# Performance work log

Hardware: AMD Instinct MI355X
Metric: run time of the kernel (lower is better)

Reference implementation:

```python
import jax, jax.numpy as jnp
import numpy as np
from jax.scipy.special import logsumexp

NEG_INF = -1e9


def _lstm(x, wih, whh, bih, bhh):
    # x: [B, L, D] -> (hs [B, L, H], h_last [B, H]); PyTorch gate order i,f,g,o
    B = x.shape[0]
    H = whh.shape[1]
    def step(carry, xt):
        h, c = carry
        g = xt @ wih.T + h @ whh.T + bih + bhh
        i, f, gg, o = jnp.split(g, 4, axis=-1)
        c = jax.nn.sigmoid(f) * c + jax.nn.sigmoid(i) * jnp.tanh(gg)
        h = jax.nn.sigmoid(o) * jnp.tanh(c)
        return (h, c), h
    init = (jnp.zeros((B, H), x.dtype), jnp.zeros((B, H), x.dtype))
    (hT, _), hs = jax.lax.scan(step, init, jnp.swapaxes(x, 0, 1))
    return jnp.swapaxes(hs, 0, 1), hT


def _forward(word_ids, char_ids, mask, tags, p):
    (word_emb, char_emb_cnn, conv_w3, conv_b3, conv_w5, conv_b5, conv_w7, conv_b7,
     char_emb_lstm, cl_wih_f, cl_whh_f, cl_bih_f, cl_bhh_f,
     cl_wih_b, cl_whh_b, cl_bih_b, cl_bhh_b,
     fuse_w, fuse_b,
     ctx_wih_f, ctx_whh_f, ctx_bih_f, ctx_bhh_f,
     ctx_wih_b, ctx_whh_b, ctx_bih_b, ctx_bhh_b,
     attn_w, attn_b, attn_v, emis_w, emis_b,
     crf_start, crf_end, crf_trans) = p
    B, T = word_ids.shape
    Wc = char_ids.shape[2]
    we = word_emb[word_ids]                                    # [B,T,200]
    cids = char_ids.reshape(B * T, Wc)
    # --- Char CNN branch: conv1d(relu) + max-over-time per kernel size ---
    ce = jnp.swapaxes(char_emb_cnn[cids], 1, 2)                # [BT,30,W]
    feats = []
    for w, b in ((conv_w3, conv_b3), (conv_w5, conv_b5), (conv_w7, conv_b7)):
        k = w.shape[-1]
        y = jax.lax.conv_general_dilated(ce, w, (1,), [(k // 2, k // 2)],
                                         dimension_numbers=('NCW', 'OIW', 'NCW'))
        feats.append(jnp.max(jax.nn.relu(y + b[None, :, None]), axis=2))
    cnn_feat = jnp.concatenate(feats, axis=1).reshape(B, T, -1)    # [B,T,96]
    # --- Char BiLSTM branch: final hidden states of both directions ---
    cel = char_emb_lstm[cids]                                  # [BT,W,30]
    _, hf = _lstm(cel, cl_wih_f, cl_whh_f, cl_bih_f, cl_bhh_f)
    _, hb = _lstm(cel[:, ::-1], cl_wih_b, cl_whh_b, cl_bih_b, cl_bhh_b)
    lstm_feat = jnp.concatenate([hf, hb], axis=1).reshape(B, T, -1)  # [B,T,100]
    # --- Fusion (dropout is identity in eval) ---
    combined = jnp.concatenate([we, cnn_feat, lstm_feat], axis=-1)   # [B,T,396]
    fused = jax.nn.relu(combined @ fuse_w.T + fuse_b)                # [B,T,200]
    # --- Context BiLSTM ---
    hs_f, _ = _lstm(fused, ctx_wih_f, ctx_whh_f, ctx_bih_f, ctx_bhh_f)
    hs_b, _ = _lstm(fused[:, ::-1], ctx_wih_b, ctx_whh_b, ctx_bih_b, ctx_bhh_b)
    H = jnp.concatenate([hs_f, hs_b[:, ::-1]], axis=-1)              # [B,T,256]
    # --- Token attention ---
    scores = jnp.tanh(H @ attn_w.T + attn_b) @ attn_v                # [B,T]
    scores = jnp.where(mask, scores, NEG_INF)
    H = H * jax.nn.softmax(scores, axis=1)[..., None]
    emis = H @ emis_w.T + emis_b                                     # [B,T,K]
    # --- CRF negative mean log-likelihood (time-major) ---
    em = jnp.swapaxes(emis, 0, 1)                                    # [T,B,K]
    m = jnp.swapaxes(mask, 0, 1).astype(em.dtype)                    # [T,B]
    tg = jnp.swapaxes(tags, 0, 1)                                    # [T,B]
    barange = jnp.arange(B)
    emit = jnp.take_along_axis(em, tg[:, :, None], axis=2)[:, :, 0]  # [T,B]
    trans_sc = crf_trans[tg[:-1], tg[1:]]                            # [T-1,B]
    num = crf_start[tg[0]] + emit[0] + jnp.sum((trans_sc + emit[1:]) * m[1:], axis=0)
    last_idx = m.sum(axis=0).astype(jnp.int32) - 1
    num = num + crf_end[tg[last_idx, barange]]
    def crf_step(alpha, inp):
        e_t, m_t = inp
        nxt = logsumexp(alpha[:, :, None] + crf_trans[None] + e_t[:, None, :], axis=1)
        return jnp.where(m_t[:, None] > 0, nxt, alpha), None
    alpha, _ = jax.lax.scan(crf_step, crf_start + em[0], (em[1:], m[1:]))
    logZ = logsumexp(alpha + crf_end, axis=1)                        # [B]
    return -(num - logZ).mean()


def setup_inputs() -> dict:
    key = jax.random.key(0)
    ks = iter(jax.random.split(key, 64))
    def rn(shape, s=0.1):
        return jax.random.normal(next(ks), shape, jnp.float32) * s
    B, T, Wc, V, Cv, K = 64, 256, 16, 100000, 100, 9
    return dict(
        word_ids=jax.random.randint(next(ks), (B, T), 0, V),
        char_ids=jax.random.randint(next(ks), (B, T, Wc), 0, Cv),
        mask=jnp.ones((B, T), bool),
        tags=jax.random.randint(next(ks), (B, T), 0, K),
        word_emb=rn((V, 200)),
        char_emb_cnn=rn((Cv, 30)),
        conv_w3=rn((32, 30, 3)), conv_b3=rn((32,)),
        conv_w5=rn((32, 30, 5)), conv_b5=rn((32,)),
        conv_w7=rn((32, 30, 7)), conv_b7=rn((32,)),
        char_emb_lstm=rn((Cv, 30)),
        cl_wih_f=rn((200, 30)), cl_whh_f=rn((200, 50)), cl_bih_f=rn((200,)), cl_bhh_f=rn((200,)),
        cl_wih_b=rn((200, 30)), cl_whh_b=rn((200, 50)), cl_bih_b=rn((200,)), cl_bhh_b=rn((200,)),
        fuse_w=rn((200, 396)), fuse_b=rn((200,)),
        ctx_wih_f=rn((512, 200)), ctx_whh_f=rn((512, 128)), ctx_bih_f=rn((512,)), ctx_bhh_f=rn((512,)),
        ctx_wih_b=rn((512, 200)), ctx_whh_b=rn((512, 128)), ctx_bih_b=rn((512,)), ctx_bhh_b=rn((512,)),
        attn_w=rn((256, 256)), attn_b=rn((256,)), attn_v=rn((256,)),
        emis_w=rn((K, 256)), emis_b=rn((K,)),
        crf_start=rn((K,)), crf_end=rn((K,)), crf_trans=rn((K, K)),
    )


def reference(word_ids, char_ids, mask, tags, word_emb, char_emb_cnn, conv_w3, conv_b3, conv_w5, conv_b5, conv_w7, conv_b7, char_emb_lstm, cl_wih_f, cl_whh_f, cl_bih_f, cl_bhh_f, cl_wih_b, cl_whh_b, cl_bih_b, cl_bhh_b, fuse_w, fuse_b, ctx_wih_f, ctx_whh_f, ctx_bih_f, ctx_bhh_f, ctx_wih_b, ctx_whh_b, ctx_bih_b, ctx_bhh_b, attn_w, attn_b, attn_v, emis_w, emis_b, crf_start, crf_end, crf_trans):
    p = (word_emb, char_emb_cnn, conv_w3, conv_b3, conv_w5, conv_b5, conv_w7, conv_b7,
         char_emb_lstm, cl_wih_f, cl_whh_f, cl_bih_f, cl_bhh_f,
         cl_wih_b, cl_whh_b, cl_bih_b, cl_bhh_b,
         fuse_w, fuse_b,
         ctx_wih_f, ctx_whh_f, ctx_bih_f, ctx_bhh_f,
         ctx_wih_b, ctx_whh_b, ctx_bih_b, ctx_bhh_b,
         attn_w, attn_b, attn_v, emis_w, emis_b,
         crf_start, crf_end, crf_trans)
    return _forward(word_ids, char_ids, mask, tags, p)
```

## Files before the change

kernel.cpp:

```cpp
#include <hip/hip_runtime.h>
#include <hip/hip_fp16.h>

#define NB_B 64
#define NT 256
#define NWC 16

__device__ __forceinline__ float sigf(float x){ return 1.0f/(1.0f + __expf(-x)); }
__device__ __forceinline__ float tanhf_(float x){ return 1.0f - 2.0f/(__expf(2.0f*x)+1.0f); }

typedef _Float16 h2_t __attribute__((ext_vector_type(2)));

__device__ __forceinline__ float dot2f(unsigned int w, unsigned int x, float acc){
#if __has_builtin(__builtin_amdgcn_fdot2)
  return __builtin_amdgcn_fdot2(__builtin_bit_cast(h2_t, w), __builtin_bit_cast(h2_t, x), acc, false);
#else
  h2_t a = __builtin_bit_cast(h2_t, w), b = __builtin_bit_cast(h2_t, x);
  return acc + (float)a[0]*(float)b[0] + (float)a[1]*(float)b[1];
#endif
}

__device__ __forceinline__ unsigned int packh2(float a, float b){
  return ((unsigned int)__half_as_ushort(__float2half(a))) |
         (((unsigned int)__half_as_ushort(__float2half(b))) << 16);
}


__global__ void k_transpose(const float* __restrict__ src, float* __restrict__ dst, int R, int C){
  int idx = blockIdx.x*256 + threadIdx.x;
  if (idx < R*C){ int r = idx / C, c = idx % C; dst[c*R + r] = src[idx]; }
}

__global__ void k_prep_ctx(const float* __restrict__ wih_f, const float* __restrict__ whh_f,
                           const float* __restrict__ bih_f, const float* __restrict__ bhh_f,
                           const float* __restrict__ wih_b, const float* __restrict__ whh_b,
                           const float* __restrict__ bih_b, const float* __restrict__ bhh_b,
                           unsigned int* __restrict__ wihP, unsigned int* __restrict__ whhQ,
                           float* __restrict__ biasc){
  int idx = blockIdx.x*256 + threadIdx.x;
  const int NIH = 2*100*512, NHH = 2*16*512*4;
  if (idx < NIH){
    int dir = idx / (100*512); int r = idx % (100*512); int k = r >> 9; int j = r & 511;
    const float* wih = dir ? wih_b : wih_f;
    wihP[idx] = packh2(wih[j*200 + 2*k], wih[j*200 + 2*k + 1]);
  } else if (idx < NIH + NHH){
    int i2 = idx - NIH;
    int dir = i2 / 32768; int r = i2 % 32768;
    int k4 = r / 2048; int r2 = r % 2048; int j = r2 >> 2; int e = r2 & 3;
    const float* whh = dir ? whh_b : whh_f;
    whhQ[i2] = packh2(whh[j*128 + 8*k4 + 2*e], whh[j*128 + 8*k4 + 2*e + 1]);
  } else if (idx < NIH + NHH + 1024){
    int i2 = idx - NIH - NHH; int dir = i2 >> 9; int j = i2 & 511;
    biasc[i2] = dir ? (bih_b[j] + bhh_b[j]) : (bih_f[j] + bhh_f[j]);
  }
}

__global__ void k_prep_P4(const float* __restrict__ emb,
                          const float* __restrict__ wih_f, const float* __restrict__ bih_f, const float* __restrict__ bhh_f,
                          const float* __restrict__ wih_b, const float* __restrict__ bih_b, const float* __restrict__ bhh_b,
                          float4* __restrict__ P4){
  int idx = blockIdx.x*256 + threadIdx.x;
  if (idx >= 10000) return;
  int dir = idx / 5000; int r = idx % 5000; int c = r / 50; int u = r % 50;
  const float* wih = dir ? wih_b : wih_f;
  const float* bih = dir ? bih_b : bih_f;
  const float* bhh = dir ? bhh_b : bhh_f;
  float g4[4];
  #pragma unroll
  for (int gt = 0; gt < 4; gt++){
    int j = gt*50 + u;
    float acc = bih[j] + bhh[j];
    for (int k = 0; k < 30; k++) acc += emb[c*30 + k] * wih[j*30 + k];
    g4[gt] = acc;
  }
  P4[idx] = make_float4(g4[0], g4[1], g4[2], g4[3]);
}

__global__ void k_prep_whh2(const float* __restrict__ whh_f, const float* __restrict__ whh_b,
                            unsigned int* __restrict__ W2){
  int idx = blockIdx.x*256 + threadIdx.x;
  if (idx >= 10000) return;
  int dir = idx / 5000; int r = idx % 5000;
  int u = r / 100; int r2 = r % 100; int gt = r2 / 25; int k = r2 % 25;
  const float* whh = dir ? whh_b : whh_f;
  int j = gt*50 + u;
  W2[idx] = packh2(whh[j*50 + 2*k], whh[j*50 + 2*k + 1]);
}

__global__ void k_prep_Q(const float* __restrict__ emb, const float* __restrict__ w3,
                         const float* __restrict__ w5, const float* __restrict__ w7,
                         float* __restrict__ Q){
  int idx = blockIdx.x*256 + threadIdx.x;
  if (idx >= 48000) return;
  const float* w; int ks, r;
  if (idx < 9600){ w = w3; ks = 3; r = idx; }
  else if (idx < 25600){ w = w5; ks = 5; r = idx - 9600; }
  else { w = w7; ks = 7; r = idx - 25600; }
  int t = r / 3200; int o = (r / 100) % 32; int c = r % 100;
  float acc = 0.f;
  for (int i = 0; i < 30; i++) acc += emb[c*30 + i] * w[(o*30 + i)*ks + t];
  Q[idx] = acc;
}


__global__ void k_gather(const int* __restrict__ word_ids, const float* __restrict__ word_emb,
                         float* __restrict__ combined){
  int idx = blockIdx.x*256 + threadIdx.x;
  if (idx >= NB_B*NT*200) return;
  int bt = idx / 200; int k = idx - bt*200;
  combined[bt*396 + k] = word_emb[(long)word_ids[bt]*200 + k];
}

template<int KS>
__global__ __launch_bounds__(512) void k_cnn2(const int* __restrict__ char_ids,
                                              const float* __restrict__ Qg,
                                              const float* __restrict__ bias,
                                              float* __restrict__ combined,
                                              int outoff){
  constexpr int PAD = KS/2;
  const int tid = threadIdx.x;
  __shared__ float Qlds[KS*3200];
  for (int idx = tid; idx < KS*3200; idx += 512){
    int t = idx / 3200; int r = idx - t*3200; int cc = r >> 5; int oo = r & 31;
    Qlds[idx] = Qg[(t*32 + oo)*100 + cc];
  }
  __syncthreads();
  const int o    = tid & 31;
  const int word = blockIdx.x*16 + ((tid >> 6) << 1) + ((tid >> 5) & 1);
  int ch[16];
  #pragma unroll
  for (int p = 0; p < 16; p++) ch[p] = char_ids[word*16 + p];
  float m = -1e30f;
  #pragma unroll
  for (int p = 0; p < 16; p++){
    float acc = 0.f;
    #pragma unroll
    for (int t = 0; t < KS; t++){
      int pp = p + t - PAD;
      if (pp >= 0 && pp < 16) acc += Qlds[(t*100 + ch[pp])*32 + o];
    }
    m = fmaxf(m, acc);
  }
  combined[(long)word*396 + 200 + outoff + o] = fmaxf(m + bias[o], 0.f);
}

__global__ __launch_bounds__(320, 2) void k_char_lstm(const int* __restrict__ char_ids,
                                                      const float4* __restrict__ P4,
                                                      const unsigned int* __restrict__ W2,
                                                      float* __restrict__ combined){
  const int lane = threadIdx.x & 63;
  const int g10  = __builtin_amdgcn_readfirstlane(threadIdx.x >> 6);
  const int word = blockIdx.x*64 + lane;
  const int dir  = blockIdx.y;
  const float4* __restrict__ P4d = P4 + dir*5000;
  const unsigned int* __restrict__ W2d = W2 + dir*5000 + g10*1000;

  __shared__ unsigned int hbuf[2][64*27];

  int ch[16];
  #pragma unroll
  for (int p = 0; p < 16; p++) ch[p] = char_ids[word*16 + p];

  float c[10], hval[10];
  #pragma unroll
  for (int u = 0; u < 10; u++){ c[u] = 0.f; hval[u] = 0.f; }
  for (int i = threadIdx.x; i < 64*27; i += 320) hbuf[0][i] = 0u;
  __syncthreads();

  #pragma unroll 1
  for (int t = 0; t < 16; t++){
    const int p = t & 1;
    const int cid = ch[dir ? (15 - t) : t];
    float4 pg[10];
    #pragma unroll
    for (int u = 0; u < 10; u++) pg[u] = P4d[cid*50 + g10*10 + u];
    unsigned int hp[25];
    #pragma unroll
    for (int k = 0; k < 25; k++) hp[k] = hbuf[p][lane*27 + k];
    #pragma unroll 2
    for (int u = 0; u < 10; u++){
      const unsigned int* __restrict__ wr = W2d + u*100;
      float ai = pg[u].x, af = pg[u].y, ag = pg[u].z, ao = pg[u].w;
      #pragma unroll
      for (int k = 0; k < 25; k++){
        ai = dot2f(wr[k],      hp[k], ai);
        af = dot2f(wr[25 + k], hp[k], af);
        ag = dot2f(wr[50 + k], hp[k], ag);
        ao = dot2f(wr[75 + k], hp[k], ao);
      }
      c[u] = sigf(af)*c[u] + sigf(ai)*tanhf_(ag);
      hval[u] = sigf(ao)*tanhf_(c[u]);
    }
    #pragma unroll
    for (int i = 0; i < 5; i++)
      hbuf[1-p][lane*27 + g10*5 + i] = packh2(hval[2*i], hval[2*i+1]);
    __syncthreads();
  }
  #pragma unroll
  for (int u = 0; u < 10; u++)
    combined[(long)word*396 + 296 + dir*50 + g10*10 + u] = hval[u];
}

__global__ __launch_bounds__(256) void k_fuse(const float* __restrict__ combined,
                                              const float* __restrict__ wFT,
                                              const float* __restrict__ fb,
                                              float* __restrict__ fused){
  int tid = threadIdx.x; int base = blockIdx.x*4;
  __shared__ float rows[4*396];
  for (int idx = tid; idx < 4*396; idx += 256) rows[idx] = combined[(long)base*396 + idx];
  __syncthreads();
  if (tid < 200){
    float a0=0.f, a1=0.f, a2=0.f, a3=0.f;
    #pragma unroll 4
    for (int k = 0; k < 396; k++){
      float w = wFT[k*200 + tid];
      a0 += w*rows[k]; a1 += w*rows[396+k]; a2 += w*rows[792+k]; a3 += w*rows[1188+k];
    }
    float bb = fb[tid];
    fused[(base+0)*200 + tid] = fmaxf(a0 + bb, 0.f);
    fused[(base+1)*200 + tid] = fmaxf(a1 + bb, 0.f);
    fused[(base+2)*200 + tid] = fmaxf(a2 + bb, 0.f);
    fused[(base+3)*200 + tid] = fmaxf(a3 + bb, 0.f);
  }
}

__global__ __launch_bounds__(512) void k_gx(const float* __restrict__ fused,
                                            const unsigned int* __restrict__ wihP,
                                            const float* __restrict__ biasc,
                                            __half* __restrict__ Gx){
  const int dir = blockIdx.y, j = threadIdx.x;
  const int base = blockIdx.x*8;
  __shared__ __align__(16) unsigned int xh[8*100];
  for (int idx = j; idx < 800; idx += 512){
    int r = idx / 100, k = idx - r*100;
    const float2* fr2 = (const float2*)(fused + (long)(base + r)*200);
    float2 v = fr2[k];
    xh[r*100 + k] = packh2(v.x, v.y);
  }
  __syncthreads();
  float acc[8];
  float bj = biasc[dir*512 + j];
  #pragma unroll
  for (int r = 0; r < 8; r++) acc[r] = bj;
  const unsigned int* wp = wihP + dir*(100*512) + j;
  #pragma unroll 1
  for (int kk = 0; kk < 25; kk++){
    unsigned int w0 = wp[(4*kk+0)*512];
    unsigned int w1 = wp[(4*kk+1)*512];
    unsigned int w2 = wp[(4*kk+2)*512];
    unsigned int w3 = wp[(4*kk+3)*512];
    #pragma unroll
    for (int r = 0; r < 8; r++){
      uint4 xv = *(const uint4*)&xh[r*100 + kk*4];
      float a = acc[r];
      a = dot2f(w0, xv.x, a);
      a = dot2f(w1, xv.y, a);
      a = dot2f(w2, xv.z, a);
      a = dot2f(w3, xv.w, a);
      acc[r] = a;
    }
  }
  #pragma unroll
  for (int r = 0; r < 8; r++)
    Gx[((long)dir*16384 + base + r)*512 + j] = __float2half(acc[r]);
}

__global__ __launch_bounds__(512) void k_ctx_rec(const __half* __restrict__ Gx,
                                                 const uint4* __restrict__ whhQ,
                                                 __half* __restrict__ H){
  const int b = blockIdx.x, dir = blockIdx.y, j = threadIdx.x;
  __shared__ __align__(16) unsigned int hh[64];
  __shared__ float gs[512];
  float c = 0.f;
  if (j < 64) hh[j] = 0u;
  __syncthreads();
  const __half* gx_base = Gx + ((long)dir*16384 + b*256)*512;
  const uint4* wq = whhQ + dir*(16*512) + j;

  #pragma unroll 1
  for (int t = 0; t < 256; t++){
    int tsrc = dir ? (255 - t) : t;
    float acc = __half2float(gx_base[(long)tsrc*512 + j]);
    const uint4* hq = (const uint4*)hh;
    #pragma unroll
    for (int k4 = 0; k4 < 16; k4++){
      uint4 w = wq[k4*512];
      uint4 hv = hq[k4];
      acc = dot2f(w.x, hv.x, acc);
      acc = dot2f(w.y, hv.y, acc);
      acc = dot2f(w.z, hv.z, acc);
      acc = dot2f(w.w, hv.w, acc);
    }
    gs[j] = acc;
    __syncthreads();
    if (j < 128){
      float gi = gs[j], gf = gs[j+128], gg = gs[j+256], go = gs[j+384];
      c = sigf(gf)*c + sigf(gi)*tanhf_(gg);
      float hv = sigf(go)*tanhf_(c);
      H[((long)b*256 + tsrc)*256 + dir*128 + j] = __float2half(hv);
      ((unsigned short*)hh)[j] = __half_as_ushort(__float2half(hv));
    }
    __syncthreads();
  }
}


__global__ __launch_bounds__(256) void k_attn(const __half* __restrict__ H,
                                              const float* __restrict__ attnT,
                                              const float* __restrict__ attn_b,
                                              const float* __restrict__ attn_v,
                                              float* __restrict__ scores){
  int tid = threadIdx.x; int base = blockIdx.x*4;
  __shared__ float rows[4*256];
  __shared__ float red[4*256];
  for (int idx = tid; idx < 1024; idx += 256) rows[idx] = __half2float(H[(long)base*256 + idx]);
  __syncthreads();
  float a0=0.f, a1=0.f, a2=0.f, a3=0.f;
  #pragma unroll 4
  for (int k = 0; k < 256; k++){
    float w = attnT[k*256 + tid];
    a0 += w*rows[k]; a1 += w*rows[256+k]; a2 += w*rows[512+k]; a3 += w*rows[768+k];
  }
  float ab = attn_b[tid], av = attn_v[tid];
  red[tid]       = tanhf_(a0 + ab)*av;
  red[256 + tid] = tanhf_(a1 + ab)*av;
  red[512 + tid] = tanhf_(a2 + ab)*av;
  red[768 + tid] = tanhf_(a3 + ab)*av;
  __syncthreads();
  for (int s = 128; s > 0; s >>= 1){
    if (tid < s){
      red[tid] += red[tid+s]; red[256+tid] += red[256+tid+s];
      red[512+tid] += red[512+tid+s]; red[768+tid] += red[768+tid+s];
    }
    __syncthreads();
  }
  if (tid < 4) scores[base + tid] = red[tid*256];
}

__global__ __launch_bounds__(256) void k_softmax(float* __restrict__ scores){
  int b = blockIdx.x, tid = threadIdx.x;
  __shared__ float red[256];
  float s = scores[b*256 + tid];
  red[tid] = s; __syncthreads();
  for (int st = 128; st > 0; st >>= 1){ if (tid < st) red[tid] = fmaxf(red[tid], red[tid+st]); __syncthreads(); }
  float m = red[0]; __syncthreads();
  float e = __expf(s - m);
  red[tid] = e; __syncthreads();
  for (int st = 128; st > 0; st >>= 1){ if (tid < st) red[tid] += red[tid+st]; __syncthreads(); }
  float inv = 1.0f / red[0];
  scores[b*256 + tid] = e * inv;
}

__global__ __launch_bounds__(256) void k_emis(const __half* __restrict__ H, const float* __restrict__ scores,
                                              const float* __restrict__ emis_w, const float* __restrict__ emis_b,
                                              float* __restrict__ emis){
  int tid = threadIdx.x; int base = blockIdx.x*4;
  int r = tid >> 6, j = tid & 63;
  __shared__ float rows[4*256];
  for (int idx = tid; idx < 1024; idx += 256) rows[idx] = __half2float(H[(long)base*256 + idx]);
  __syncthreads();
  if (j < 9){
    float acc = 0.f;
    #pragma unroll 4
    for (int k = 0; k < 256; k++) acc += rows[r*256 + k] * emis_w[j*256 + k];
    int tok = base + r;
    emis[tok*9 + j] = scores[tok]*acc + emis_b[j];
  }
}


__global__ __launch_bounds__(64) void k_crf(const float* __restrict__ emis, const float* __restrict__ trans,
                                            const float* __restrict__ startv, const float* __restrict__ endv,
                                            float* __restrict__ logZ){
  int b = blockIdx.x; int j = threadIdx.x;
  bool act = (j < 9);
  float alpha = act ? (startv[j] + emis[(b*256)*9 + j]) : -1e30f;
  float trow[9];
  #pragma unroll
  for (int i = 0; i < 9; i++) trow[i] = act ? trans[i*9 + j] : 0.f;
  for (int t = 1; t < 256; t++){
    float v[9];
    #pragma unroll
    for (int i = 0; i < 9; i++) v[i] = __shfl(alpha, i) + trow[i];
    float m = v[0];
    #pragma unroll
    for (int i = 1; i < 9; i++) m = fmaxf(m, v[i]);
    float ssum = 0.f;
    #pragma unroll
    for (int i = 0; i < 9; i++) ssum += expf(v[i] - m);
    float e = act ? emis[(b*256 + t)*9 + j] : 0.f;
    alpha = m + logf(ssum) + e;
  }
  float v = act ? (alpha + endv[j]) : -1e30f;
  float vv[9];
  float m = -1e30f;
  #pragma unroll
  for (int i = 0; i < 9; i++){ vv[i] = __shfl(v, i); m = fmaxf(m, vv[i]); }
  float ssum = 0.f;
  #pragma unroll
  for (int i = 0; i < 9; i++) ssum += expf(vv[i] - m);
  if (j == 0) logZ[b] = m + logf(ssum);
}

__global__ __launch_bounds__(256) void k_num(const int* __restrict__ tags, const float* __restrict__ emis,
                                             const float* __restrict__ trans, const float* __restrict__ startv,
                                             const float* __restrict__ endv, float* __restrict__ num){
  int b = blockIdx.x, t = threadIdx.x;
  int tg = tags[b*256 + t];
  float v = emis[(b*256 + t)*9 + tg];
  if (t > 0) v += trans[tags[b*256 + t - 1]*9 + tg];
  __shared__ float red[256];
  red[t] = v; __syncthreads();
  for (int s = 128; s > 0; s >>= 1){ if (t < s) red[t] += red[t+s]; __syncthreads(); }
  if (t == 0) num[b] = red[0] + startv[tags[b*256]] + endv[tags[b*256 + 255]];
}

__global__ __launch_bounds__(64) void k_final(const float* __restrict__ logZ, const float* __restrict__ num,
                                              float* __restrict__ out){
  int b = threadIdx.x;
  float v = logZ[b] - num[b];
  for (int s = 32; s > 0; s >>= 1) v += __shfl_down(v, s);
  if (b == 0) out[0] = v * (1.0f/64.0f);
}

__global__ void k_diag(float* __restrict__ out, float ws_mb){
  if (threadIdx.x == 0) out[0] = -ws_mb;
}


extern "C" void kernel_launch(void* const* d_in, const int* in_sizes, int n_in,
                              void* d_out, int out_size, void* d_ws, size_t ws_size,
                              hipStream_t stream) {
  const int*   word_ids   = (const int*)  d_in[0];
  const int*   char_ids   = (const int*)  d_in[1];
  const int*   tags       = (const int*)  d_in[3];
  const float* word_emb   = (const float*)d_in[4];
  const float* emb_cnn    = (const float*)d_in[5];
  const float* conv_w3    = (const float*)d_in[6];
  const float* conv_b3    = (const float*)d_in[7];
  const float* conv_w5    = (const float*)d_in[8];
  const float* conv_b5    = (const float*)d_in[9];
  const float* conv_w7    = (const float*)d_in[10];
  const float* conv_b7    = (const float*)d_in[11];
  const float* emb_lstm   = (const float*)d_in[12];
  const float* cl_wih_f   = (const float*)d_in[13];
  const float* cl_whh_f   = (const float*)d_in[14];
  const float* cl_bih_f   = (const float*)d_in[15];
  const float* cl_bhh_f   = (const float*)d_in[16];
  const float* cl_wih_b   = (const float*)d_in[17];
  const float* cl_whh_b   = (const float*)d_in[18];
  const float* cl_bih_b   = (const float*)d_in[19];
  const float* cl_bhh_b   = (const float*)d_in[20];
  const float* fuse_w     = (const float*)d_in[21];
  const float* fuse_b     = (const float*)d_in[22];
  const float* ctx_wih_f  = (const float*)d_in[23];
  const float* ctx_whh_f  = (const float*)d_in[24];
  const float* ctx_bih_f  = (const float*)d_in[25];
  const float* ctx_bhh_f  = (const float*)d_in[26];
  const float* ctx_wih_b  = (const float*)d_in[27];
  const float* ctx_whh_b  = (const float*)d_in[28];
  const float* ctx_bih_b  = (const float*)d_in[29];
  const float* ctx_bhh_b  = (const float*)d_in[30];
  const float* attn_w     = (const float*)d_in[31];
  const float* attn_b     = (const float*)d_in[32];
  const float* attn_v     = (const float*)d_in[33];
  const float* emis_w     = (const float*)d_in[34];
  const float* emis_b     = (const float*)d_in[35];
  const float* crf_start  = (const float*)d_in[36];
  const float* crf_end    = (const float*)d_in[37];
  const float* crf_trans  = (const float*)d_in[38];
  float* out = (float*)d_out;
  float* ws  = (float*)d_ws;

  const size_t OFF_A      = 0;
  const size_t OFF_FUSED  = 8388608;
  const size_t OFF_SCORES = 11665408;
  const size_t OFF_EMIS   = 11681792;
  const size_t OFF_WIHP   = 11829248;
  const size_t OFF_WHHQ   = 11931648;
  const size_t OFF_BIASC  = 11997184;
  const size_t OFF_P4     = 11998208;
  const size_t OFF_Q      = 12038208;
  const size_t OFF_W2     = 12086208;
  const size_t OFF_WFT    = 12096208;
  const size_t OFF_ATTNT  = 12175408;
  const size_t OFF_NUM    = 12240944;
  const size_t OFF_LOGZ   = 12241008;
  const size_t TOTAL_FLOATS = 12241072;

  if (ws_size < TOTAL_FLOATS * sizeof(float)) {
    k_diag<<<1, 64, 0, stream>>>(out, (float)((double)ws_size / (1024.0*1024.0)));
    return;
  }

  float* combined = ws + OFF_A;
  __half* Gx      = (__half*)(ws + OFF_A);
  float* fused    = ws + OFF_FUSED;
  __half* H       = (__half*)(ws + OFF_FUSED);
  float* scores   = ws + OFF_SCORES;
  float* emis     = ws + OFF_EMIS;
  unsigned int* wihP = (unsigned int*)(ws + OFF_WIHP);
  unsigned int* whhQ = (unsigned int*)(ws + OFF_WHHQ);
  float* biasc    = ws + OFF_BIASC;
  float4* P4      = (float4*)(ws + OFF_P4);
  float* Q        = ws + OFF_Q;
  unsigned int* W2 = (unsigned int*)(ws + OFF_W2);
  float* wFT      = ws + OFF_WFT;
  float* attnT    = ws + OFF_ATTNT;
  float* num      = ws + OFF_NUM;
  float* logZ     = ws + OFF_LOGZ;

  k_transpose<<<(200*396 + 255)/256, 256, 0, stream>>>(fuse_w, wFT, 200, 396);
  k_transpose<<<(256*256 + 255)/256, 256, 0, stream>>>(attn_w, attnT, 256, 256);
  k_prep_ctx<<<(2*100*512 + 2*16*512*4 + 1024 + 255)/256, 256, 0, stream>>>(
      ctx_wih_f, ctx_whh_f, ctx_bih_f, ctx_bhh_f,
      ctx_wih_b, ctx_whh_b, ctx_bih_b, ctx_bhh_b, wihP, whhQ, biasc);
  k_prep_P4<<<(10000 + 255)/256, 256, 0, stream>>>(
      emb_lstm, cl_wih_f, cl_bih_f, cl_bhh_f, cl_wih_b, cl_bih_b, cl_bhh_b, P4);
  k_prep_whh2<<<(10000 + 255)/256, 256, 0, stream>>>(cl_whh_f, cl_whh_b, W2);
  k_prep_Q<<<(48000 + 255)/256, 256, 0, stream>>>(emb_cnn, conv_w3, conv_w5, conv_w7, Q);

  k_gather<<<(NB_B*NT*200 + 255)/256, 256, 0, stream>>>(word_ids, word_emb, combined);
  k_cnn2<3><<<NB_B*NT/16, 512, 0, stream>>>(char_ids, Q,         conv_b3, combined, 0);
  k_cnn2<5><<<NB_B*NT/16, 512, 0, stream>>>(char_ids, Q + 9600,  conv_b5, combined, 32);
  k_cnn2<7><<<NB_B*NT/16, 512, 0, stream>>>(char_ids, Q + 25600, conv_b7, combined, 64);
  k_char_lstm<<<dim3(NB_B*NT/64, 2), 320, 0, stream>>>(char_ids, P4, W2, combined);
  k_fuse<<<NB_B*NT/4, 256, 0, stream>>>(combined, wFT, fuse_b, fused);

  k_gx<<<dim3(NB_B*NT/8, 2), 512, 0, stream>>>(fused, wihP, biasc, Gx);
  k_ctx_rec<<<dim3(NB_B, 2), 512, 0, stream>>>(Gx, (const uint4*)whhQ, H);

  k_attn<<<NB_B*NT/4, 256, 0, stream>>>(H, attnT, attn_b, attn_v, scores);
  k_softmax<<<NB_B, 256, 0, stream>>>(scores);
  k_emis<<<NB_B*NT/4, 256, 0, stream>>>(H, scores, emis_w, emis_b, emis);

  k_crf<<<NB_B, 64, 0, stream>>>(emis, crf_trans, crf_start, crf_end, logZ);
  k_num<<<NB_B, 256, 0, stream>>>(tags, emis, crf_trans, crf_start, crf_end, num);
  k_final<<<1, 64, 0, stream>>>(logZ, num, out);
}
```

Baseline: 1.131 ms.

## Rewrite char BiLSTM recurrence with MFMA 16x16x32 f16 matrix ops

The char-level BiLSTM recurrence now runs on MFMA instructions instead of per-lane fdot2 loops. Each wavefront handles 16 words independently. Recurrent weights are pre-packed into padded f16 B-fragments held in registers, and the input projection table is interleaved per gate so it can seed the accumulator. Gates are redistributed through LDS per wave with no block-wide barriers. The goal is to remove the scalar dot-product cost and the syncthreads per timestep. The price is padding waste (50 to 52 units, 50 to 64 K) and extra LDS round trips.

```diff
diff --git a/kernel.cpp b/kernel.cpp
--- a/kernel.cpp
+++ b/kernel.cpp
@@ -9,6 +9,8 @@
 __device__ __forceinline__ float tanhf_(float x){ return 1.0f - 2.0f/(__expf(2.0f*x)+1.0f); }
 
 typedef _Float16 h2_t __attribute__((ext_vector_type(2)));
+typedef _Float16 f16x8 __attribute__((ext_vector_type(8)));
+typedef float    f32x4 __attribute__((ext_vector_type(4)));
 
 __device__ __forceinline__ float dot2f(unsigned int w, unsigned int x, float acc){
 #if __has_builtin(__builtin_amdgcn_fdot2)
@@ -54,36 +56,41 @@
   }
 }
 
-__global__ void k_prep_P4(const float* __restrict__ emb,
-                          const float* __restrict__ wih_f, const float* __restrict__ bih_f, const float* __restrict__ bhh_f,
-                          const float* __restrict__ wih_b, const float* __restrict__ bih_b, const float* __restrict__ bhh_b,
-                          float4* __restrict__ P4){
+__global__ void k_prep_p4i(const float* __restrict__ emb,
+                           const float* __restrict__ wih_f, const float* __restrict__ bih_f, const float* __restrict__ bhh_f,
+                           const float* __restrict__ wih_b, const float* __restrict__ bih_b, const float* __restrict__ bhh_b,
+                           float* __restrict__ P4I){
   int idx = blockIdx.x*256 + threadIdx.x;
-  if (idx >= 10000) return;
-  int dir = idx / 5000; int r = idx % 5000; int c = r / 50; int u = r % 50;
-  const float* wih = dir ? wih_b : wih_f;
-  const float* bih = dir ? bih_b : bih_f;
-  const float* bhh = dir ? bhh_b : bhh_f;
-  float g4[4];
-  #pragma unroll
-  for (int gt = 0; gt < 4; gt++){
-    int j = gt*50 + u;
+  if (idx >= 41600) return;
+  int n = idx % 208; int cd = idx / 208; int cid = cd % 100; int dir = cd / 100;
+  int u = n >> 2, g = n & 3;
+  float v = 0.f;
+  if (u < 50){
+    int j = g*50 + u;
+    const float* wih = dir ? wih_b : wih_f;
+    const float* bih = dir ? bih_b : bih_f;
+    const float* bhh = dir ? bhh_b : bhh_f;
     float acc = bih[j] + bhh[j];
-    for (int k = 0; k < 30; k++) acc += emb[c*30 + k] * wih[j*30 + k];
-    g4[gt] = acc;
-  }
-  P4[idx] = make_float4(g4[0], g4[1], g4[2], g4[3]);
-}
-
-__global__ void k_prep_whh2(const float* __restrict__ whh_f, const float* __restrict__ whh_b,
-                            unsigned int* __restrict__ W2){
+    for (int k = 0; k < 30; k++) acc += emb[cid*30 + k] * wih[j*30 + k];
+    v = acc;
+  }
+  P4I[idx] = v;
+}
+
+__global__ void k_prep_wb(const float* __restrict__ whh_f, const float* __restrict__ whh_b,
+                          unsigned short* __restrict__ WB){
   int idx = blockIdx.x*256 + threadIdx.x;
-  if (idx >= 10000) return;
-  int dir = idx / 5000; int r = idx % 5000;
-  int u = r / 100; int r2 = r % 100; int gt = r2 / 25; int k = r2 % 25;
+  if (idx >= 26624) return;
+  int e = idx & 7; int l = (idx >> 3) & 63;
+  int dirf = idx >> 9;
+  int dir = dirf / 26; int fr = dirf % 26;
+  int tau = fr >> 1, kh = fr & 1;
+  int n = 16*tau + (l & 15);
+  int u = n >> 2, g = n & 3;
+  int k = kh*32 + (l >> 4)*8 + e;
   const float* whh = dir ? whh_b : whh_f;
-  int j = gt*50 + u;
-  W2[idx] = packh2(whh[j*50 + 2*k], whh[j*50 + 2*k + 1]);
+  float v = (u < 50 && k < 50) ? whh[(g*50 + u)*50 + k] : 0.f;
+  WB[idx] = __half_as_ushort(__float2half(v));
 }
 
 __global__ void k_prep_Q(const float* __restrict__ emb, const float* __restrict__ w3,
@@ -143,61 +150,128 @@
   combined[(long)word*396 + 200 + outoff + o] = fmaxf(m + bias[o], 0.f);
 }
 
-__global__ __launch_bounds__(320, 2) void k_char_lstm(const int* __restrict__ char_ids,
-                                                      const float4* __restrict__ P4,
-                                                      const unsigned int* __restrict__ W2,
+__global__ __launch_bounds__(256, 2) void k_char_lstm(const int* __restrict__ char_ids,
+                                                      const float* __restrict__ P4I,
+                                                      const unsigned short* __restrict__ WB,
                                                       float* __restrict__ combined){
-  const int lane = threadIdx.x & 63;
-  const int g10  = __builtin_amdgcn_readfirstlane(threadIdx.x >> 6);
-  const int word = blockIdx.x*64 + lane;
+  const int tid  = threadIdx.x;
+  const int wv   = tid >> 6;
+  const int lane = tid & 63;
+  const int c15  = lane & 15;
+  const int grp  = lane >> 4;
   const int dir  = blockIdx.y;
-  const float4* __restrict__ P4d = P4 + dir*5000;
-  const unsigned int* __restrict__ W2d = W2 + dir*5000 + g10*1000;
-
-  __shared__ unsigned int hbuf[2][64*27];
-
-  int ch[16];
-  #pragma unroll
-  for (int p = 0; p < 16; p++) ch[p] = char_ids[word*16 + p];
-
-  float c[10], hval[10];
-  #pragma unroll
-  for (int u = 0; u < 10; u++){ c[u] = 0.f; hval[u] = 0.f; }
-  for (int i = threadIdx.x; i < 64*27; i += 320) hbuf[0][i] = 0u;
-  __syncthreads();
+  const int wbase = blockIdx.x*64 + wv*16;
+
+  __shared__ __align__(16) float          glds_all[4][16*124];
+  __shared__ __align__(16) unsigned short hlds_all[4][16*72];
+  __shared__ int                          chl_all[4][16*16];
+  float*          glds = glds_all[wv];
+  unsigned short* hlds = hlds_all[wv];
+  int*            chl  = chl_all[wv];
+
+  f16x8 bf[26];
+  {
+    const unsigned short* wb = WB + ((long)dir*26)*512 + lane*8;
+    #pragma unroll
+    for (int f = 0; f < 26; f++)
+      bf[f] = *reinterpret_cast<const f16x8*>(wb + f*512);
+  }
+
+  for (int i = lane; i < 256; i += 64){
+    int w = i >> 4, t = i & 15;
+    chl[i] = char_ids[(long)(wbase + w)*16 + t];
+  }
+  for (int i = lane; i < 16*72; i += 64) hlds[i] = 0;
+  __syncthreads();
+
+  float cc[13], hfin[13];
+  #pragma unroll
+  for (int q = 0; q < 13; q++){ cc[q] = 0.f; hfin[q] = 0.f; }
+
+  const float* pbase = P4I + (long)dir*20800 + c15;
 
   #pragma unroll 1
   for (int t = 0; t < 16; t++){
-    const int p = t & 1;
-    const int cid = ch[dir ? (15 - t) : t];
-    float4 pg[10];
-    #pragma unroll
-    for (int u = 0; u < 10; u++) pg[u] = P4d[cid*50 + g10*10 + u];
-    unsigned int hp[25];
-    #pragma unroll
-    for (int k = 0; k < 25; k++) hp[k] = hbuf[p][lane*27 + k];
-    #pragma unroll 2
-    for (int u = 0; u < 10; u++){
-      const unsigned int* __restrict__ wr = W2d + u*100;
-      float ai = pg[u].x, af = pg[u].y, ag = pg[u].z, ao = pg[u].w;
+    const int tt = dir ? (15 - t) : t;
+    int cid0 = chl[(grp*4+0)*16 + tt];
+    int cid1 = chl[(grp*4+1)*16 + tt];
+    int cid2 = chl[(grp*4+2)*16 + tt];
+    int cid3 = chl[(grp*4+3)*16 + tt];
+    const float* p0 = pbase + cid0*208;
+    const float* p1 = pbase + cid1*208;
+    const float* p2 = pbase + cid2*208;
+    const float* p3 = pbase + cid3*208;
+
+    f16x8 a0 = *reinterpret_cast<const f16x8*>(&hlds[c15*72 + grp*8]);
+    f16x8 a1 = *reinterpret_cast<const f16x8*>(&hlds[c15*72 + 32 + grp*8]);
+
+    {
+      f32x4 acc[7];
       #pragma unroll
-      for (int k = 0; k < 25; k++){
-        ai = dot2f(wr[k],      hp[k], ai);
-        af = dot2f(wr[25 + k], hp[k], af);
-        ag = dot2f(wr[50 + k], hp[k], ag);
-        ao = dot2f(wr[75 + k], hp[k], ao);
+      for (int tau = 0; tau < 7; tau++){
+        f32x4 ci;
+        ci[0] = p0[16*tau]; ci[1] = p1[16*tau]; ci[2] = p2[16*tau]; ci[3] = p3[16*tau];
+        f32x4 m0 = __builtin_amdgcn_mfma_f32_16x16x32_f16(a0, bf[2*tau+0], ci, 0, 0, 0);
+        acc[tau]  = __builtin_amdgcn_mfma_f32_16x16x32_f16(a1, bf[2*tau+1], m0, 0, 0, 0);
       }
-      c[u] = sigf(af)*c[u] + sigf(ai)*tanhf_(ag);
-      hval[u] = sigf(ao)*tanhf_(c[u]);
-    }
-    #pragma unroll
-    for (int i = 0; i < 5; i++)
-      hbuf[1-p][lane*27 + g10*5 + i] = packh2(hval[2*i], hval[2*i+1]);
-    __syncthreads();
-  }
-  #pragma unroll
-  for (int u = 0; u < 10; u++)
-    combined[(long)word*396 + 296 + dir*50 + g10*10 + u] = hval[u];
+      #pragma unroll
+      for (int tau = 0; tau < 7; tau++)
+        #pragma unroll
+        for (int r = 0; r < 4; r++)
+          glds[(grp*4+r)*124 + tau*16 + c15] = acc[tau][r];
+      #pragma unroll
+      for (int q = 0; q < 7; q++){
+        int u = grp*7 + q;
+        f32x4 gq = *reinterpret_cast<const f32x4*>(&glds[c15*124 + 4*u]);
+        float cn = sigf(gq[1])*cc[q] + sigf(gq[0])*tanhf_(gq[2]);
+        cc[q] = cn;
+        float hv = sigf(gq[3])*tanhf_(cn);
+        hfin[q] = hv;
+        hlds[c15*72 + u] = __half_as_ushort(__float2half(hv));
+      }
+    }
+    {
+      f32x4 acc[6];
+      #pragma unroll
+      for (int s = 0; s < 6; s++){
+        int tau = 7 + s;
+        f32x4 ci;
+        ci[0] = p0[16*tau]; ci[1] = p1[16*tau]; ci[2] = p2[16*tau]; ci[3] = p3[16*tau];
+        f32x4 m0 = __builtin_amdgcn_mfma_f32_16x16x32_f16(a0, bf[2*tau+0], ci, 0, 0, 0);
+        acc[s]    = __builtin_amdgcn_mfma_f32_16x16x32_f16(a1, bf[2*tau+1], m0, 0, 0, 0);
+      }
+      #pragma unroll
+      for (int s = 0; s < 6; s++)
+        #pragma unroll
+        for (int r = 0; r < 4; r++)
+          glds[(grp*4+r)*124 + s*16 + c15] = acc[s][r];
+      #pragma unroll
+      for (int q = 0; q < 6; q++){
+        int u = 28 + grp*6 + q;
+        if (u < 50){
+          f32x4 gq = *reinterpret_cast<const f32x4*>(&glds[c15*124 + 4*u - 112]);
+          float cn = sigf(gq[1])*cc[7+q] + sigf(gq[0])*tanhf_(gq[2]);
+          cc[7+q] = cn;
+          float hv = sigf(gq[3])*tanhf_(cn);
+          hfin[7+q] = hv;
+          hlds[c15*72 + u] = __half_as_ushort(__float2half(hv));
+        }
+      }
+    }
+  }
+
+  #pragma unroll
+  for (int q = 0; q < 7; q++) glds[c15*50 + grp*7 + q] = hfin[q];
+  #pragma unroll
+  for (int q = 0; q < 6; q++){
+    int u = 28 + grp*6 + q;
+    if (u < 50) glds[c15*50 + u] = hfin[7+q];
+  }
+  __builtin_amdgcn_s_waitcnt(0);
+  for (int i = lane; i < 800; i += 64){
+    int w = i / 50; int j = i - w*50;
+    combined[(long)(wbase + w)*396 + 296 + dir*50 + j] = glds[i];
+  }
 }
 
 __global__ __launch_bounds__(256) void k_fuse(const float* __restrict__ combined,
@@ -478,14 +552,14 @@
   const size_t OFF_WIHP   = 11829248;
   const size_t OFF_WHHQ   = 11931648;
   const size_t OFF_BIASC  = 11997184;
-  const size_t OFF_P4     = 11998208;
-  const size_t OFF_Q      = 12038208;
-  const size_t OFF_W2     = 12086208;
-  const size_t OFF_WFT    = 12096208;
-  const size_t OFF_ATTNT  = 12175408;
-  const size_t OFF_NUM    = 12240944;
-  const size_t OFF_LOGZ   = 12241008;
-  const size_t TOTAL_FLOATS = 12241072;
+  const size_t OFF_P4I    = 11998208;
+  const size_t OFF_Q      = 12039808;
+  const size_t OFF_WB     = 12087808;
+  const size_t OFF_WFT    = 12101120;
+  const size_t OFF_ATTNT  = 12180320;
+  const size_t OFF_NUM    = 12245856;
+  const size_t OFF_LOGZ   = 12245920;
+  const size_t TOTAL_FLOATS = 12245984;
 
   if (ws_size < TOTAL_FLOATS * sizeof(float)) {
     k_diag<<<1, 64, 0, stream>>>(out, (float)((double)ws_size / (1024.0*1024.0)));
@@ -501,9 +575,9 @@
   unsigned int* wihP = (unsigned int*)(ws + OFF_WIHP);
   unsigned int* whhQ = (unsigned int*)(ws + OFF_WHHQ);
   float* biasc    = ws + OFF_BIASC;
-  float4* P4      = (float4*)(ws + OFF_P4);
+  float* P4I      = ws + OFF_P4I;
   float* Q        = ws + OFF_Q;
-  unsigned int* W2 = (unsigned int*)(ws + OFF_W2);
+  unsigned short* WBu = (unsigned short*)(ws + OFF_WB);
   float* wFT      = ws + OFF_WFT;
   float* attnT    = ws + OFF_ATTNT;
   float* num      = ws + OFF_NUM;
@@ -514,16 +588,16 @@
   k_prep_ctx<<<(2*100*512 + 2*16*512*4 + 1024 + 255)/256, 256, 0, stream>>>(
       ctx_wih_f, ctx_whh_f, ctx_bih_f, ctx_bhh_f,
       ctx_wih_b, ctx_whh_b, ctx_bih_b, ctx_bhh_b, wihP, whhQ, biasc);
-  k_prep_P4<<<(10000 + 255)/256, 256, 0, stream>>>(
-      emb_lstm, cl_wih_f, cl_bih_f, cl_bhh_f, cl_wih_b, cl_bih_b, cl_bhh_b, P4);
-  k_prep_whh2<<<(10000 + 255)/256, 256, 0, stream>>>(cl_whh_f, cl_whh_b, W2);
+  k_prep_p4i<<<(41600 + 255)/256, 256, 0, stream>>>(
+      emb_lstm, cl_wih_f, cl_bih_f, cl_bhh_f, cl_wih_b, cl_bih_b, cl_bhh_b, P4I);
+  k_prep_wb<<<(26624 + 255)/256, 256, 0, stream>>>(cl_whh_f, cl_whh_b, WBu);
   k_prep_Q<<<(48000 + 255)/256, 256, 0, stream>>>(emb_cnn, conv_w3, conv_w5, conv_w7, Q);
 
   k_gather<<<(NB_B*NT*200 + 255)/256, 256, 0, stream>>>(word_ids, word_emb, combined);
   k_cnn2<3><<<NB_B*NT/16, 512, 0, stream>>>(char_ids, Q,         conv_b3, combined, 0);
   k_cnn2<5><<<NB_B*NT/16, 512, 0, stream>>>(char_ids, Q + 9600,  conv_b5, combined, 32);
   k_cnn2<7><<<NB_B*NT/16, 512, 0, stream>>>(char_ids, Q + 25600, conv_b7, combined, 64);
-  k_char_lstm<<<dim3(NB_B*NT/64, 2), 320, 0, stream>>>(char_ids, P4, W2, combined);
+  k_char_lstm<<<dim3(NB_B*NT/64, 2), 256, 0, stream>>>(char_ids, P4I, WBu, combined);
   k_fuse<<<NB_B*NT/4, 256, 0, stream>>>(combined, wFT, fuse_b, fused);
 
   k_gx<<<dim3(NB_B*NT/8, 2), 512, 0, stream>>>(fused, wihP, biasc, Gx);
```

Result: faster. 929.1 us (-17.9%).
